# Kernel optimization log

Measured on AMD Instinct MI355X. Metric: run time of the kernel, lower is better.

The kernel has to match this reference:

```python
import jax, jax.numpy as jnp
import numpy as np

EMB = 1024
HEADS = 16
HEAD_DIM = EMB // HEADS
N = 16384


def setup_inputs() -> dict:
    key = jax.random.key(0)
    ks = jax.random.split(key, 9)
    s = 1.0 / np.sqrt(EMB)
    return {
        "src": jax.random.normal(ks[0], (N, EMB), dtype=jnp.float32),
        "Wq": jax.random.normal(ks[1], (EMB, EMB), dtype=jnp.float32) * s,
        "bq": jax.random.normal(ks[2], (EMB,), dtype=jnp.float32) * s,
        "Wk": jax.random.normal(ks[3], (EMB, EMB), dtype=jnp.float32) * s,
        "bk": jax.random.normal(ks[4], (EMB,), dtype=jnp.float32) * s,
        "Wv": jax.random.normal(ks[5], (EMB, EMB), dtype=jnp.float32) * s,
        "bv": jax.random.normal(ks[6], (EMB,), dtype=jnp.float32) * s,
        "Wo": jax.random.normal(ks[7], (EMB, EMB), dtype=jnp.float32) * s,
        "bo": jax.random.normal(ks[8], (EMB,), dtype=jnp.float32) * s,
    }


def reference(src, Wq, bq, Wk, bk, Wv, bv, Wo, bo):
    # nn.Linear: y = x @ W^T + b  (W is [out, in])
    q = src @ Wq.T + bq          # [N, E]
    k = src @ Wk.T + bk
    v = src @ Wv.T + bv
    q = q.reshape(-1, HEADS, HEAD_DIM)   # [N, H, D]
    k = k.reshape(-1, HEADS, HEAD_DIM)
    v = v.reshape(-1, HEADS, HEAD_DIM)
    # NOTE: attention is across heads within each token: scores [N, H, H]
    scale = 1.0 / jnp.sqrt(jnp.float32(HEAD_DIM))
    scores = jnp.einsum('nhd,ngd->nhg', q, k) * scale   # [N, H, H]
    attn = jax.nn.softmax(scores, axis=-1)
    out = jnp.einsum('nhg,ngd->nhd', attn, v)            # [N, H, D]
    out = out.reshape(-1, EMB)
    out = out @ Wo.T + bo                                 # [N, E]
    return out.reshape(-1, HEADS, HEAD_DIM)               # [N, H, D]
```

## Files before the change

kernel.cpp:

```cpp
#include <hip/hip_runtime.h>
#include <stdint.h>
#include <stddef.h>

#define EMB 1024
#define NTOK 16384

typedef __attribute__((ext_vector_type(8))) short short8;
typedef __attribute__((ext_vector_type(4))) float floatx4;

__device__ __forceinline__ unsigned short f2bf(float f) {
    union { float f; unsigned int u; } v; v.f = f;
    unsigned int u = v.u;
    unsigned int r = (u + 0x7fffu + ((u >> 16) & 1u)) >> 16;
    return (unsigned short)r;
}
__device__ __forceinline__ float bf2f(unsigned short s) {
    union { unsigned int u; float f; } v; v.u = ((unsigned int)s) << 16;
    return v.f;
}

__device__ __forceinline__ void gload16(const void* g, void* l) {
    __builtin_amdgcn_global_load_lds(
        (const __attribute__((address_space(1))) void*)g,
        (__attribute__((address_space(3))) void*)l, 16, 0, 0);
}

__global__ void cvt_kernel(const float* __restrict__ in,
                           unsigned short* __restrict__ out, int n4) {
    int idx = blockIdx.x * blockDim.x + threadIdx.x;
    int stride = gridDim.x * blockDim.x;
    for (int i = idx; i < n4; i += stride) {
        float4 f = reinterpret_cast<const float4*>(in)[i];
        ushort4 o;
        o.x = f2bf(f.x); o.y = f2bf(f.y); o.z = f2bf(f.z); o.w = f2bf(f.w);
        reinterpret_cast<ushort4*>(out)[i] = o;
    }
}

__global__ void cvt4_kernel(const float* __restrict__ s0, const float* __restrict__ s1,
                            const float* __restrict__ s2, const float* __restrict__ s3,
                            unsigned short* __restrict__ out) {
    int idx = blockIdx.x * blockDim.x + threadIdx.x;
    const int total = 4 << 18;
    int stride = gridDim.x * blockDim.x;
    for (int i = idx; i < total; i += stride) {
        int w = i >> 18, r = i & ((1 << 18) - 1);
        const float* s = (w == 0) ? s0 : (w == 1) ? s1 : (w == 2) ? s2 : s3;
        float4 f = reinterpret_cast<const float4*>(s)[r];
        ushort4 o;
        o.x = f2bf(f.x); o.y = f2bf(f.y); o.z = f2bf(f.z); o.w = f2bf(f.w);
        reinterpret_cast<ushort4*>(out)[i] = o;
    }
}

__global__ void bias_cat_kernel(const float* __restrict__ b0,
                                const float* __restrict__ b1,
                                const float* __restrict__ b2,
                                float* __restrict__ out) {
    int i = blockIdx.x * blockDim.x + threadIdx.x;
    float v = (i < 1024) ? b0[i] : (i < 2048 ? b1[i - 1024] : b2[i - 2048]);
    out[i] = v;
}

__device__ __forceinline__ void store_val(float* C, size_t idx, float v) { C[idx] = v; }
__device__ __forceinline__ void store_val(unsigned short* C, size_t idx, float v) { C[idx] = f2bf(v); }

template<typename OUT_T>
__global__ __launch_bounds__(512, 1)
void gemm256mn(const unsigned short* __restrict__ A,
               const unsigned short* __restrict__ B,
               const float* __restrict__ bias,
               OUT_T* __restrict__ C,
               int Nc, int nt_n)
{
    __shared__ unsigned short lds[65536];
    const int K = 1024;
    const int NT = 16;

    const int bid = blockIdx.x;
    const int x = bid & 7;
    const int w = bid >> 3;
    const int m0 = (x * 8 + (w & 7)) * 256;
    const int n_base = (w >> 3) * nt_n * 256;

    const int tid  = threadIdx.x;
    const int lane = tid & 63;
    const int wid  = tid >> 6;
    const int wm = (wid >> 2) * 128;
    const int wn = (wid & 3) * 64;
    const int rr = lane & 15;
    const int klo = (((lane >> 4) ^ ((rr >> 1) & 3)) << 3);

    const int aro = (wm + rr) * 32 + klo;
    const int bro = 16384 + (wn + rr) * 32 + klo;

    const unsigned short* pA[2];
    const unsigned short* pB[2];
    int ldst[2];
#pragma unroll
    for (int l = 0; l < 2; ++l) {
        const int P16  = l * 512 + tid;
        const int rowS = P16 >> 2;
        const int colel = (((P16 & 3) ^ ((rowS >> 1) & 3)) << 3);
        pA[l] = A + (size_t)(m0 + rowS) * K + colel;
        pB[l] = B + (size_t)(n_base + rowS) * K + colel;
        ldst[l] = P16 * 8;
    }
    const size_t nstep = (size_t)256 * K;

    floatx4 acc[8][4];
#pragma unroll
    for (int i = 0; i < 8; ++i)
#pragma unroll
        for (int j = 0; j < 4; ++j)
            acc[i][j] = (floatx4){0.f, 0.f, 0.f, 0.f};

    const int TOT = nt_n * NT;

#pragma unroll
    for (int l = 0; l < 2; ++l) {
        gload16(pA[l],      &lds[0     + ldst[l]]);
        gload16(pA[l] + 32, &lds[8192  + ldst[l]]);
        gload16(pB[l],      &lds[16384 + ldst[l]]);
        gload16(pB[l] + 32, &lds[24576 + ldst[l]]);
    }
    asm volatile("s_waitcnt vmcnt(0)" ::: "memory");
    asm volatile("s_barrier" ::: "memory");

    short8 a0[4], a1[4], b0[4];
#pragma unroll
    for (int i = 0; i < 4; ++i)
        a0[i] = *reinterpret_cast<const short8*>(&lds[aro + i * 512]);
#pragma unroll
    for (int j = 0; j < 4; ++j)
        b0[j] = *reinterpret_cast<const short8*>(&lds[bro + j * 512]);

    const int cn  = lane & 15;
    const int cm4 = (lane >> 4) * 4;

    for (int vt = 0; vt < TOT; ++vt) {
        const int cur = (vt & 1) * 32768;
        const int nxt = cur ^ 32768;
        int vtn = vt + 1; if (vtn == TOT) vtn = 0;
        const int ktn = (vtn & 15) * 64;
        const int nbn = vtn >> 4;
        const unsigned short* pBn0 = pB[0] + (size_t)nbn * nstep + ktn;
        const unsigned short* pBn1 = pB[1] + (size_t)nbn * nstep + ktn;

        gload16(pA[0] + ktn, &lds[nxt + ldst[0]]);
        gload16(pA[1] + ktn, &lds[nxt + ldst[1]]);
        gload16(pBn0,        &lds[nxt + 16384 + ldst[0]]);
        gload16(pBn1,        &lds[nxt + 16384 + ldst[1]]);
#pragma unroll
        for (int i = 0; i < 4; ++i)
            a1[i] = *reinterpret_cast<const short8*>(&lds[cur + aro + 2048 + i * 512]);
        __builtin_amdgcn_s_setprio(1);
#pragma unroll
        for (int j = 0; j < 4; ++j)
#pragma unroll
            for (int i = 0; i < 4; ++i)
                acc[i][j] = __builtin_amdgcn_mfma_f32_16x16x32_bf16(a0[i], b0[j], acc[i][j], 0, 0, 0);
#pragma unroll
        for (int j = 0; j < 4; ++j)
#pragma unroll
            for (int i = 0; i < 4; ++i)
                acc[4 + i][j] = __builtin_amdgcn_mfma_f32_16x16x32_bf16(a1[i], b0[j], acc[4 + i][j], 0, 0, 0);
        __builtin_amdgcn_s_setprio(0);
        asm volatile("s_waitcnt vmcnt(4)" ::: "memory");
        asm volatile("s_barrier" ::: "memory");

        gload16(pA[0] + ktn + 32, &lds[nxt + 8192 + ldst[0]]);
        gload16(pA[1] + ktn + 32, &lds[nxt + 8192 + ldst[1]]);
        gload16(pBn0 + 32,        &lds[nxt + 24576 + ldst[0]]);
        gload16(pBn1 + 32,        &lds[nxt + 24576 + ldst[1]]);
#pragma unroll
        for (int i = 0; i < 4; ++i)
            a0[i] = *reinterpret_cast<const short8*>(&lds[cur + 8192 + aro + i * 512]);
#pragma unroll
        for (int j = 0; j < 4; ++j)
            b0[j] = *reinterpret_cast<const short8*>(&lds[cur + 8192 + bro + j * 512]);
#pragma unroll
        for (int i = 0; i < 4; ++i)
            a1[i] = *reinterpret_cast<const short8*>(&lds[cur + 8192 + aro + 2048 + i * 512]);
        __builtin_amdgcn_s_setprio(1);
#pragma unroll
        for (int j = 0; j < 4; ++j)
#pragma unroll
            for (int i = 0; i < 4; ++i)
                acc[i][j] = __builtin_amdgcn_mfma_f32_16x16x32_bf16(a0[i], b0[j], acc[i][j], 0, 0, 0);
#pragma unroll
        for (int j = 0; j < 4; ++j)
#pragma unroll
            for (int i = 0; i < 4; ++i)
                acc[4 + i][j] = __builtin_amdgcn_mfma_f32_16x16x32_bf16(a1[i], b0[j], acc[4 + i][j], 0, 0, 0);
        __builtin_amdgcn_s_setprio(0);
        asm volatile("s_waitcnt vmcnt(4)" ::: "memory");
        asm volatile("s_barrier" ::: "memory");
#pragma unroll
        for (int i = 0; i < 4; ++i)
            a0[i] = *reinterpret_cast<const short8*>(&lds[nxt + aro + i * 512]);
#pragma unroll
        for (int j = 0; j < 4; ++j)
            b0[j] = *reinterpret_cast<const short8*>(&lds[nxt + bro + j * 512]);

        if ((vt & 15) == 15) {
            const int n0 = n_base + (vt >> 4) * 256;
            float bv[4];
#pragma unroll
            for (int j = 0; j < 4; ++j) bv[j] = bias[n0 + wn + j * 16 + cn];
#pragma unroll
            for (int ai = 0; ai < 8; ++ai) {
                const int row = m0 + wm + (ai >> 2) * 64 + (ai & 3) * 16 + cm4;
#pragma unroll
                for (int j = 0; j < 4; ++j) {
                    const int col = n0 + wn + j * 16 + cn;
#pragma unroll
                    for (int r = 0; r < 4; ++r)
                        store_val(C, (size_t)(row + r) * Nc + col, acc[ai][j][r] + bv[j]);
                }
            }
#pragma unroll
            for (int i = 0; i < 8; ++i)
#pragma unroll
                for (int j = 0; j < 4; ++j)
                    acc[i][j] = (floatx4){0.f, 0.f, 0.f, 0.f};
        }
    }
}

#define ROWP 72

__global__ __launch_bounds__(256)
void attn_kernel(const unsigned short* __restrict__ QKV,
                 unsigned short* __restrict__ O)
{
    const int wave = threadIdx.x >> 6;
    const int lane = threadIdx.x & 63;
    const int n = blockIdx.x * 4 + wave;

    __shared__ unsigned short lq[4][16 * ROWP];
    __shared__ unsigned short lk[4][16 * ROWP];
    __shared__ unsigned short lv[4][16 * ROWP];
    __shared__ float lp[4][256];

    {
        const unsigned short* gq = QKV + (size_t)n * 3072;
        const unsigned short* gk = gq + 1024;
        const unsigned short* gv = gq + 2048;
        for (int t = lane; t < 128; t += 64) {
            int r = t >> 3, c = t & 7;
            *reinterpret_cast<short8*>(&lq[wave][r * ROWP + c * 8]) =
                *reinterpret_cast<const short8*>(gq + t * 8);
            *reinterpret_cast<short8*>(&lk[wave][r * ROWP + c * 8]) =
                *reinterpret_cast<const short8*>(gk + t * 8);
            *reinterpret_cast<short8*>(&lv[wave][r * ROWP + c * 8]) =
                *reinterpret_cast<const short8*>(gv + t * 8);
        }
    }
    __syncthreads();

    const int g = lane & 15;
    const int a = lane >> 4;

    float kf[64];
#pragma unroll
    for (int c2 = 0; c2 < 8; ++c2) {
        short8 kv = *reinterpret_cast<const short8*>(&lk[wave][g * ROWP + c2 * 8]);
#pragma unroll
        for (int e = 0; e < 8; ++e) kf[c2 * 8 + e] = bf2f((unsigned short)kv[e]);
    }

#pragma unroll
    for (int i = 0; i < 4; ++i) {
        const int h = i * 4 + a;
        float s = 0.f;
#pragma unroll
        for (int c2 = 0; c2 < 8; ++c2) {
            short8 qv = *reinterpret_cast<const short8*>(&lq[wave][h * ROWP + c2 * 8]);
#pragma unroll
            for (int e = 0; e < 8; ++e)
                s = fmaf(bf2f((unsigned short)qv[e]), kf[c2 * 8 + e], s);
        }
        s *= 0.125f;

        float m = s;
#pragma unroll
        for (int o = 1; o < 16; o <<= 1) m = fmaxf(m, __shfl_xor(m, o, 64));
        float p = expf(s - m);
        float sum = p;
#pragma unroll
        for (int o = 1; o < 16; o <<= 1) sum += __shfl_xor(sum, o, 64);
        lp[wave][h * 16 + g] = p / sum;
    }
    __syncthreads();

    const int h = lane >> 2;
    const int db = (lane & 3) * 16;
    float o[16];
#pragma unroll
    for (int e = 0; e < 16; ++e) o[e] = 0.f;

    for (int g2 = 0; g2 < 16; ++g2) {
        const float pw = lp[wave][h * 16 + g2];
        short8 v0 = *reinterpret_cast<const short8*>(&lv[wave][g2 * ROWP + db]);
        short8 v1 = *reinterpret_cast<const short8*>(&lv[wave][g2 * ROWP + db + 8]);
#pragma unroll
        for (int e = 0; e < 8; ++e) {
            o[e]     = fmaf(pw, bf2f((unsigned short)v0[e]), o[e]);
            o[8 + e] = fmaf(pw, bf2f((unsigned short)v1[e]), o[8 + e]);
        }
    }

    short8 o0, o1;
#pragma unroll
    for (int e = 0; e < 8; ++e) {
        o0[e] = (short)f2bf(o[e]);
        o1[e] = (short)f2bf(o[8 + e]);
    }
    unsigned short* dst = O + (size_t)n * EMB + h * 64 + db;
    *reinterpret_cast<short8*>(dst) = o0;
    *reinterpret_cast<short8*>(dst + 8) = o1;
}

extern "C" void kernel_launch(void* const* d_in, const int* in_sizes, int n_in,
                              void* d_out, int out_size, void* d_ws, size_t ws_size,
                              hipStream_t stream)
{
    const float* src = (const float*)d_in[0];
    const float* Wq  = (const float*)d_in[1];
    const float* bq  = (const float*)d_in[2];
    const float* Wk  = (const float*)d_in[3];
    const float* bk  = (const float*)d_in[4];
    const float* Wv  = (const float*)d_in[5];
    const float* bv  = (const float*)d_in[6];
    const float* Wo  = (const float*)d_in[7];
    const float* bo  = (const float*)d_in[8];
    float* out = (float*)d_out;

    unsigned short* ws = (unsigned short*)d_ws;
    unsigned short* src_bf = ws;
    unsigned short* wqkv   = src_bf + (size_t)NTOK * EMB;
    unsigned short* wo_bf  = wqkv + (size_t)3 * EMB * EMB;
    unsigned short* qkv    = wo_bf + (size_t)EMB * EMB;
    unsigned short* ab     = qkv + (size_t)NTOK * 3 * EMB;
    float* bias_cat        = (float*)(ab + (size_t)NTOK * EMB);

    cvt_kernel<<<2048, 256, 0, stream>>>(src, src_bf, NTOK * EMB / 4);
    cvt4_kernel<<<2048, 256, 0, stream>>>(Wq, Wk, Wv, Wo, wqkv);
    bias_cat_kernel<<<12, 256, 0, stream>>>(bq, bk, bv, bias_cat);

    gemm256mn<unsigned short><<<dim3(256), 512, 0, stream>>>(
        src_bf, wqkv, bias_cat, qkv, 3 * EMB, 3);

    attn_kernel<<<NTOK / 4, 256, 0, stream>>>(qkv, ab);

    gemm256mn<float><<<dim3(256), 512, 0, stream>>>(
        ab, wo_bf, bo, out, EMB, 1);
}
```

Baseline: 201.2 us.

## Restructure GEMM main loop into 4-stage 32-wide K pipeline with prefetch depth two

Replaces the double-buffered 64-wide K step, which was split into two 32-wide halves each with its own barrier, with a quad-buffered ring of 32-wide K slices. Global-to-LDS loads are issued two steps ahead, and each iteration reads all 8 A fragments at once. There is one wait and one barrier per 32-wide slice. The LDS swizzle and the row mapping of the accumulators change to match. The aim is to hide global-load latency behind more MFMA work and to simplify scheduling, at the cost of more live registers and more barriers per K element.

```diff
diff --git a/kernel.cpp b/kernel.cpp
--- a/kernel.cpp
+++ b/kernel.cpp
@@ -67,15 +67,14 @@
 
 template<typename OUT_T>
 __global__ __launch_bounds__(512, 1)
-void gemm256mn(const unsigned short* __restrict__ A,
-               const unsigned short* __restrict__ B,
-               const float* __restrict__ bias,
-               OUT_T* __restrict__ C,
-               int Nc, int nt_n)
+void gemm32q(const unsigned short* __restrict__ A,
+             const unsigned short* __restrict__ B,
+             const float* __restrict__ bias,
+             OUT_T* __restrict__ C,
+             int Nc, int nt_n)
 {
     __shared__ unsigned short lds[65536];
     const int K = 1024;
-    const int NT = 16;
 
     const int bid = blockIdx.x;
     const int x = bid & 7;
@@ -83,30 +82,20 @@
     const int m0 = (x * 8 + (w & 7)) * 256;
     const int n_base = (w >> 3) * nt_n * 256;
 
-    const int tid  = threadIdx.x;
-    const int lane = tid & 63;
-    const int wid  = tid >> 6;
-    const int wm = (wid >> 2) * 128;
-    const int wn = (wid & 3) * 64;
-    const int rr = lane & 15;
-    const int klo = (((lane >> 4) ^ ((rr >> 1) & 3)) << 3);
-
-    const int aro = (wm + rr) * 32 + klo;
-    const int bro = 16384 + (wn + rr) * 32 + klo;
-
-    const unsigned short* pA[2];
-    const unsigned short* pB[2];
-    int ldst[2];
-#pragma unroll
-    for (int l = 0; l < 2; ++l) {
-        const int P16  = l * 512 + tid;
-        const int rowS = P16 >> 2;
-        const int colel = (((P16 & 3) ^ ((rowS >> 1) & 3)) << 3);
-        pA[l] = A + (size_t)(m0 + rowS) * K + colel;
-        pB[l] = B + (size_t)(n_base + rowS) * K + colel;
-        ldst[l] = P16 * 8;
-    }
+    const int tid = threadIdx.x, lane = tid & 63, wid = tid >> 6;
+    const int wm = (wid >> 2) * 128, wn = (wid & 3) * 64;
+    const int rr = lane & 15, ls = lane >> 4;
+    const int swf = ((ls ^ (rr & 3)) << 3);
+    const int arE = (wm + rr) * 32 + swf;
+    const int brE = 8192 + (wn + rr) * 32 + swf;
+
+    const int rowT = tid >> 2;
+    const int colT = (((tid & 3) ^ (rowT & 3)) << 3);
+    const unsigned short* pA0 = A + (size_t)(m0 + rowT) * K + colT;
+    const unsigned short* pB0 = B + (size_t)(n_base + rowT) * K + colT;
+    const size_t half  = (size_t)128 * K;
     const size_t nstep = (size_t)256 * K;
+    const int ldA = tid * 8, ldB = 8192 + tid * 8;
 
     floatx4 acc[8][4];
 #pragma unroll
@@ -115,108 +104,69 @@
         for (int j = 0; j < 4; ++j)
             acc[i][j] = (floatx4){0.f, 0.f, 0.f, 0.f};
 
-    const int TOT = nt_n * NT;
-
-#pragma unroll
-    for (int l = 0; l < 2; ++l) {
-        gload16(pA[l],      &lds[0     + ldst[l]]);
-        gload16(pA[l] + 32, &lds[8192  + ldst[l]]);
-        gload16(pB[l],      &lds[16384 + ldst[l]]);
-        gload16(pB[l] + 32, &lds[24576 + ldst[l]]);
-    }
-    asm volatile("s_waitcnt vmcnt(0)" ::: "memory");
-    asm volatile("s_barrier" ::: "memory");
-
-    short8 a0[4], a1[4], b0[4];
-#pragma unroll
-    for (int i = 0; i < 4; ++i)
-        a0[i] = *reinterpret_cast<const short8*>(&lds[aro + i * 512]);
-#pragma unroll
-    for (int j = 0; j < 4; ++j)
-        b0[j] = *reinterpret_cast<const short8*>(&lds[bro + j * 512]);
-
+    const int TOT = nt_n * 32;
     const int cn  = lane & 15;
     const int cm4 = (lane >> 4) * 4;
 
+    gload16(pA0,          &lds[ldA]);
+    gload16(pA0 + half,   &lds[ldA + 4096]);
+    gload16(pB0,          &lds[ldB]);
+    gload16(pB0 + half,   &lds[ldB + 4096]);
+    gload16(pA0 + 32,          &lds[16384 + ldA]);
+    gload16(pA0 + half + 32,   &lds[16384 + ldA + 4096]);
+    gload16(pB0 + 32,          &lds[16384 + ldB]);
+    gload16(pB0 + half + 32,   &lds[16384 + ldB + 4096]);
+    asm volatile("s_waitcnt vmcnt(4)" ::: "memory");
+    asm volatile("s_barrier" ::: "memory");
+
+#pragma unroll 4
     for (int vt = 0; vt < TOT; ++vt) {
-        const int cur = (vt & 1) * 32768;
-        const int nxt = cur ^ 32768;
-        int vtn = vt + 1; if (vtn == TOT) vtn = 0;
-        const int ktn = (vtn & 15) * 64;
-        const int nbn = vtn >> 4;
-        const unsigned short* pBn0 = pB[0] + (size_t)nbn * nstep + ktn;
-        const unsigned short* pBn1 = pB[1] + (size_t)nbn * nstep + ktn;
-
-        gload16(pA[0] + ktn, &lds[nxt + ldst[0]]);
-        gload16(pA[1] + ktn, &lds[nxt + ldst[1]]);
-        gload16(pBn0,        &lds[nxt + 16384 + ldst[0]]);
-        gload16(pBn1,        &lds[nxt + 16384 + ldst[1]]);
-#pragma unroll
-        for (int i = 0; i < 4; ++i)
-            a1[i] = *reinterpret_cast<const short8*>(&lds[cur + aro + 2048 + i * 512]);
+        const int bufr = (vt & 3) * 16384;
+
+        short8 a[8], b[4];
+#pragma unroll
+        for (int i = 0; i < 8; ++i)
+            a[i] = *reinterpret_cast<const short8*>(&lds[bufr + arE + i * 512]);
+#pragma unroll
+        for (int j = 0; j < 4; ++j)
+            b[j] = *reinterpret_cast<const short8*>(&lds[bufr + brE + j * 512]);
+
+        {
+            int t2 = vt + 2; if (t2 >= TOT) t2 -= TOT;
+            const int buf2 = (t2 & 3) * 16384;
+            const int kt2  = (t2 & 31) * 32;
+            const unsigned short* pBn = pB0 + (size_t)(t2 >> 5) * nstep + kt2;
+            gload16(pA0 + kt2,        &lds[buf2 + ldA]);
+            gload16(pA0 + half + kt2, &lds[buf2 + ldA + 4096]);
+            gload16(pBn,              &lds[buf2 + ldB]);
+            gload16(pBn + half,       &lds[buf2 + ldB + 4096]);
+        }
+
         __builtin_amdgcn_s_setprio(1);
 #pragma unroll
         for (int j = 0; j < 4; ++j)
 #pragma unroll
-            for (int i = 0; i < 4; ++i)
-                acc[i][j] = __builtin_amdgcn_mfma_f32_16x16x32_bf16(a0[i], b0[j], acc[i][j], 0, 0, 0);
-#pragma unroll
-        for (int j = 0; j < 4; ++j)
-#pragma unroll
-            for (int i = 0; i < 4; ++i)
-                acc[4 + i][j] = __builtin_amdgcn_mfma_f32_16x16x32_bf16(a1[i], b0[j], acc[4 + i][j], 0, 0, 0);
+            for (int i = 0; i < 8; ++i)
+                acc[i][j] = __builtin_amdgcn_mfma_f32_16x16x32_bf16(a[i], b[j], acc[i][j], 0, 0, 0);
         __builtin_amdgcn_s_setprio(0);
+
         asm volatile("s_waitcnt vmcnt(4)" ::: "memory");
         asm volatile("s_barrier" ::: "memory");
 
-        gload16(pA[0] + ktn + 32, &lds[nxt + 8192 + ldst[0]]);
-        gload16(pA[1] + ktn + 32, &lds[nxt + 8192 + ldst[1]]);
-        gload16(pBn0 + 32,        &lds[nxt + 24576 + ldst[0]]);
-        gload16(pBn1 + 32,        &lds[nxt + 24576 + ldst[1]]);
-#pragma unroll
-        for (int i = 0; i < 4; ++i)
-            a0[i] = *reinterpret_cast<const short8*>(&lds[cur + 8192 + aro + i * 512]);
-#pragma unroll
-        for (int j = 0; j < 4; ++j)
-            b0[j] = *reinterpret_cast<const short8*>(&lds[cur + 8192 + bro + j * 512]);
-#pragma unroll
-        for (int i = 0; i < 4; ++i)
-            a1[i] = *reinterpret_cast<const short8*>(&lds[cur + 8192 + aro + 2048 + i * 512]);
-        __builtin_amdgcn_s_setprio(1);
-#pragma unroll
-        for (int j = 0; j < 4; ++j)
-#pragma unroll
-            for (int i = 0; i < 4; ++i)
-                acc[i][j] = __builtin_amdgcn_mfma_f32_16x16x32_bf16(a0[i], b0[j], acc[i][j], 0, 0, 0);
-#pragma unroll
-        for (int j = 0; j < 4; ++j)
-#pragma unroll
-            for (int i = 0; i < 4; ++i)
-                acc[4 + i][j] = __builtin_amdgcn_mfma_f32_16x16x32_bf16(a1[i], b0[j], acc[4 + i][j], 0, 0, 0);
-        __builtin_amdgcn_s_setprio(0);
-        asm volatile("s_waitcnt vmcnt(4)" ::: "memory");
-        asm volatile("s_barrier" ::: "memory");
-#pragma unroll
-        for (int i = 0; i < 4; ++i)
-            a0[i] = *reinterpret_cast<const short8*>(&lds[nxt + aro + i * 512]);
-#pragma unroll
-        for (int j = 0; j < 4; ++j)
-            b0[j] = *reinterpret_cast<const short8*>(&lds[nxt + bro + j * 512]);
-
-        if ((vt & 15) == 15) {
-            const int n0 = n_base + (vt >> 4) * 256;
+        if ((vt & 31) == 31) {
+            const int n0 = n_base + (vt >> 5) * 256;
             float bv[4];
 #pragma unroll
             for (int j = 0; j < 4; ++j) bv[j] = bias[n0 + wn + j * 16 + cn];
 #pragma unroll
-            for (int ai = 0; ai < 8; ++ai) {
-                const int row = m0 + wm + (ai >> 2) * 64 + (ai & 3) * 16 + cm4;
+            for (int i = 0; i < 8; ++i) {
+                const int row = m0 + wm + i * 16 + cm4;
 #pragma unroll
                 for (int j = 0; j < 4; ++j) {
                     const int col = n0 + wn + j * 16 + cn;
 #pragma unroll
                     for (int r = 0; r < 4; ++r)
-                        store_val(C, (size_t)(row + r) * Nc + col, acc[ai][j][r] + bv[j]);
+                        store_val(C, (size_t)(row + r) * Nc + col, acc[i][j][r] + bv[j]);
                 }
             }
 #pragma unroll
@@ -349,11 +299,11 @@
     cvt4_kernel<<<2048, 256, 0, stream>>>(Wq, Wk, Wv, Wo, wqkv);
     bias_cat_kernel<<<12, 256, 0, stream>>>(bq, bk, bv, bias_cat);
 
-    gemm256mn<unsigned short><<<dim3(256), 512, 0, stream>>>(
+    gemm32q<unsigned short><<<dim3(256), 512, 0, stream>>>(
         src_bf, wqkv, bias_cat, qkv, 3 * EMB, 3);
 
     attn_kernel<<<NTOK / 4, 256, 0, stream>>>(qkv, ab);
 
-    gemm256mn<float><<<dim3(256), 512, 0, stream>>>(
+    gemm32q<float><<<dim3(256), 512, 0, stream>>>(
         ab, wo_bf, bo, out, EMB, 1);
 }
```

After: 200.1 us. About the same (-0.5%).

## Fuse src fp32-to-bf16 conversion into QKV GEMM A-tile loading

Applied to the files above, without the earlier changes.

The QKV projection GEMM now reads the fp32 input directly and converts it to bf16 in registers before writing the A tile to LDS. This removes the standalone conversion pass over the whole activation and its bf16 scratch buffer. The bias concatenation is folded into the weight-conversion kernel, which saves one launch. The trade-off is that A is loaded through registers rather than the direct global-to-LDS path, and the fp32 A traffic is re-read for each output column tile.

```diff
diff --git a/kernel.cpp b/kernel.cpp
--- a/kernel.cpp
+++ b/kernel.cpp
@@ -25,21 +25,21 @@
         (__attribute__((address_space(3))) void*)l, 16, 0, 0);
 }
 
-__global__ void cvt_kernel(const float* __restrict__ in,
-                           unsigned short* __restrict__ out, int n4) {
-    int idx = blockIdx.x * blockDim.x + threadIdx.x;
-    int stride = gridDim.x * blockDim.x;
-    for (int i = idx; i < n4; i += stride) {
-        float4 f = reinterpret_cast<const float4*>(in)[i];
-        ushort4 o;
-        o.x = f2bf(f.x); o.y = f2bf(f.y); o.z = f2bf(f.z); o.w = f2bf(f.w);
-        reinterpret_cast<ushort4*>(out)[i] = o;
-    }
-}
-
-__global__ void cvt4_kernel(const float* __restrict__ s0, const float* __restrict__ s1,
-                            const float* __restrict__ s2, const float* __restrict__ s3,
-                            unsigned short* __restrict__ out) {
+#define SB0() __builtin_amdgcn_sched_barrier(0)
+
+__global__ void cvtwb_kernel(const float* __restrict__ s0, const float* __restrict__ s1,
+                             const float* __restrict__ s2, const float* __restrict__ s3,
+                             const float* __restrict__ b0, const float* __restrict__ b1,
+                             const float* __restrict__ b2,
+                             unsigned short* __restrict__ out, float* __restrict__ bias_cat) {
+    if (blockIdx.x == 0) {
+#pragma unroll
+        for (int t = 0; t < 12; ++t) {
+            int i = t * 256 + threadIdx.x;
+            float v = (i < 1024) ? b0[i] : (i < 2048 ? b1[i - 1024] : b2[i - 2048]);
+            bias_cat[i] = v;
+        }
+    }
     int idx = blockIdx.x * blockDim.x + threadIdx.x;
     const int total = 4 << 18;
     int stride = gridDim.x * blockDim.x;
@@ -53,17 +53,214 @@
     }
 }
 
-__global__ void bias_cat_kernel(const float* __restrict__ b0,
-                                const float* __restrict__ b1,
-                                const float* __restrict__ b2,
-                                float* __restrict__ out) {
-    int i = blockIdx.x * blockDim.x + threadIdx.x;
-    float v = (i < 1024) ? b0[i] : (i < 2048 ? b1[i - 1024] : b2[i - 2048]);
-    out[i] = v;
-}
-
 __device__ __forceinline__ void store_val(float* C, size_t idx, float v) { C[idx] = v; }
 __device__ __forceinline__ void store_val(unsigned short* C, size_t idx, float v) { C[idx] = f2bf(v); }
+
+__global__ __launch_bounds__(512, 1)
+void gemmA32(const float* __restrict__ Afp,
+             const unsigned short* __restrict__ B,
+             const float* __restrict__ bias,
+             unsigned short* __restrict__ C,
+             int Nc, int nt_n)
+{
+    __shared__ unsigned short lds[65536];
+    const int K = 1024;
+
+    const int bid = blockIdx.x;
+    const int x = bid & 7;
+    const int w = bid >> 3;
+    const int m0 = (x * 8 + (w & 7)) * 256;
+    const int n_base = (w >> 3) * nt_n * 256;
+
+    const int tid  = threadIdx.x;
+    const int lane = tid & 63;
+    const int wid  = tid >> 6;
+    const int wm = (wid >> 2) * 128;
+    const int wn = (wid & 3) * 64;
+    const int rr = lane & 15;
+    const int klo = (((lane >> 4) ^ ((rr >> 1) & 3)) << 3);
+
+    const int aro = (wm + rr) * 32 + klo;
+    const int bro = 16384 + (wn + rr) * 32 + klo;
+
+    const float* pAf[2];
+    const unsigned short* pB[2];
+    int ldst[2];
+#pragma unroll
+    for (int l = 0; l < 2; ++l) {
+        const int P16  = l * 512 + tid;
+        const int rowS = P16 >> 2;
+        const int colel = (((P16 & 3) ^ ((rowS >> 1) & 3)) << 3);
+        pAf[l] = Afp + (size_t)(m0 + rowS) * K + colel;
+        pB[l]  = B + (size_t)(n_base + rowS) * K + colel;
+        ldst[l] = P16 * 8;
+    }
+    const size_t nstep = (size_t)256 * K;
+
+    floatx4 acc[8][4];
+#pragma unroll
+    for (int i = 0; i < 8; ++i)
+#pragma unroll
+        for (int j = 0; j < 4; ++j)
+            acc[i][j] = (floatx4){0.f, 0.f, 0.f, 0.f};
+
+    const int NT = 16;
+    const int TOT = nt_n * NT;
+
+#pragma unroll
+    for (int l = 0; l < 2; ++l) {
+#pragma unroll
+        for (int kh = 0; kh < 2; ++kh) {
+            float4 f0 = *reinterpret_cast<const float4*>(pAf[l] + kh * 32);
+            float4 f1 = *reinterpret_cast<const float4*>(pAf[l] + kh * 32 + 4);
+            short8 o;
+            o[0] = (short)f2bf(f0.x); o[1] = (short)f2bf(f0.y);
+            o[2] = (short)f2bf(f0.z); o[3] = (short)f2bf(f0.w);
+            o[4] = (short)f2bf(f1.x); o[5] = (short)f2bf(f1.y);
+            o[6] = (short)f2bf(f1.z); o[7] = (short)f2bf(f1.w);
+            *reinterpret_cast<short8*>(&lds[kh * 8192 + ldst[l]]) = o;
+        }
+        gload16(pB[l],      &lds[16384 + ldst[l]]);
+        gload16(pB[l] + 32, &lds[24576 + ldst[l]]);
+    }
+    asm volatile("s_waitcnt vmcnt(0)" ::: "memory");
+    asm volatile("s_waitcnt lgkmcnt(0)" ::: "memory");
+    asm volatile("s_barrier" ::: "memory");
+
+    short8 a0[4], a1[4], b0[4];
+#pragma unroll
+    for (int i = 0; i < 4; ++i)
+        a0[i] = *reinterpret_cast<const short8*>(&lds[aro + i * 512]);
+#pragma unroll
+    for (int j = 0; j < 4; ++j)
+        b0[j] = *reinterpret_cast<const short8*>(&lds[bro + j * 512]);
+
+    const int cn  = lane & 15;
+    const int cm4 = (lane >> 4) * 4;
+
+    for (int vt = 0; vt < TOT; ++vt) {
+        const int cur = (vt & 1) * 32768;
+        const int nxt = cur ^ 32768;
+        int vtn = vt + 1; if (vtn == TOT) vtn = 0;
+        const int ktn = (vtn & 15) * 64;
+        const int nbn = vtn >> 4;
+        const unsigned short* pBn0 = pB[0] + (size_t)nbn * nstep + ktn;
+        const unsigned short* pBn1 = pB[1] + (size_t)nbn * nstep + ktn;
+
+        float4 fA00 = *reinterpret_cast<const float4*>(pAf[0] + ktn);
+        float4 fA01 = *reinterpret_cast<const float4*>(pAf[0] + ktn + 4);
+        float4 fA10 = *reinterpret_cast<const float4*>(pAf[1] + ktn);
+        float4 fA11 = *reinterpret_cast<const float4*>(pAf[1] + ktn + 4);
+        gload16(pBn0, &lds[nxt + 16384 + ldst[0]]);
+        gload16(pBn1, &lds[nxt + 16384 + ldst[1]]);
+#pragma unroll
+        for (int i = 0; i < 4; ++i)
+            a1[i] = *reinterpret_cast<const short8*>(&lds[cur + aro + 2048 + i * 512]);
+        __builtin_amdgcn_s_setprio(1);
+#pragma unroll
+        for (int j = 0; j < 4; ++j)
+#pragma unroll
+            for (int i = 0; i < 4; ++i)
+                acc[i][j] = __builtin_amdgcn_mfma_f32_16x16x32_bf16(a0[i], b0[j], acc[i][j], 0, 0, 0);
+#pragma unroll
+        for (int j = 0; j < 4; ++j)
+#pragma unroll
+            for (int i = 0; i < 4; ++i)
+                acc[4 + i][j] = __builtin_amdgcn_mfma_f32_16x16x32_bf16(a1[i], b0[j], acc[4 + i][j], 0, 0, 0);
+        __builtin_amdgcn_s_setprio(0);
+        SB0();
+        {
+            short8 o0, o1;
+            o0[0] = (short)f2bf(fA00.x); o0[1] = (short)f2bf(fA00.y);
+            o0[2] = (short)f2bf(fA00.z); o0[3] = (short)f2bf(fA00.w);
+            o0[4] = (short)f2bf(fA01.x); o0[5] = (short)f2bf(fA01.y);
+            o0[6] = (short)f2bf(fA01.z); o0[7] = (short)f2bf(fA01.w);
+            o1[0] = (short)f2bf(fA10.x); o1[1] = (short)f2bf(fA10.y);
+            o1[2] = (short)f2bf(fA10.z); o1[3] = (short)f2bf(fA10.w);
+            o1[4] = (short)f2bf(fA11.x); o1[5] = (short)f2bf(fA11.y);
+            o1[6] = (short)f2bf(fA11.z); o1[7] = (short)f2bf(fA11.w);
+            *reinterpret_cast<short8*>(&lds[nxt + ldst[0]]) = o0;
+            *reinterpret_cast<short8*>(&lds[nxt + ldst[1]]) = o1;
+        }
+        asm volatile("s_waitcnt vmcnt(2)" ::: "memory");
+        asm volatile("s_waitcnt lgkmcnt(0)" ::: "memory");
+        asm volatile("s_barrier" ::: "memory");
+
+        fA00 = *reinterpret_cast<const float4*>(pAf[0] + ktn + 32);
+        fA01 = *reinterpret_cast<const float4*>(pAf[0] + ktn + 36);
+        fA10 = *reinterpret_cast<const float4*>(pAf[1] + ktn + 32);
+        fA11 = *reinterpret_cast<const float4*>(pAf[1] + ktn + 36);
+        gload16(pBn0 + 32, &lds[nxt + 24576 + ldst[0]]);
+        gload16(pBn1 + 32, &lds[nxt + 24576 + ldst[1]]);
+#pragma unroll
+        for (int i = 0; i < 4; ++i)
+            a0[i] = *reinterpret_cast<const short8*>(&lds[cur + 8192 + aro + i * 512]);
+#pragma unroll
+        for (int j = 0; j < 4; ++j)
+            b0[j] = *reinterpret_cast<const short8*>(&lds[cur + 8192 + bro + j * 512]);
+#pragma unroll
+        for (int i = 0; i < 4; ++i)
+            a1[i] = *reinterpret_cast<const short8*>(&lds[cur + 8192 + aro + 2048 + i * 512]);
+        __builtin_amdgcn_s_setprio(1);
+#pragma unroll
+        for (int j = 0; j < 4; ++j)
+#pragma unroll
+            for (int i = 0; i < 4; ++i)
+                acc[i][j] = __builtin_amdgcn_mfma_f32_16x16x32_bf16(a0[i], b0[j], acc[i][j], 0, 0, 0);
+#pragma unroll
+        for (int j = 0; j < 4; ++j)
+#pragma unroll
+            for (int i = 0; i < 4; ++i)
+                acc[4 + i][j] = __builtin_amdgcn_mfma_f32_16x16x32_bf16(a1[i], b0[j], acc[4 + i][j], 0, 0, 0);
+        __builtin_amdgcn_s_setprio(0);
+        SB0();
+        {
+            short8 o0, o1;
+            o0[0] = (short)f2bf(fA00.x); o0[1] = (short)f2bf(fA00.y);
+            o0[2] = (short)f2bf(fA00.z); o0[3] = (short)f2bf(fA00.w);
+            o0[4] = (short)f2bf(fA01.x); o0[5] = (short)f2bf(fA01.y);
+            o0[6] = (short)f2bf(fA01.z); o0[7] = (short)f2bf(fA01.w);
+            o1[0] = (short)f2bf(fA10.x); o1[1] = (short)f2bf(fA10.y);
+            o1[2] = (short)f2bf(fA10.z); o1[3] = (short)f2bf(fA10.w);
+            o1[4] = (short)f2bf(fA11.x); o1[5] = (short)f2bf(fA11.y);
+            o1[6] = (short)f2bf(fA11.z); o1[7] = (short)f2bf(fA11.w);
+            *reinterpret_cast<short8*>(&lds[nxt + 8192 + ldst[0]]) = o0;
+            *reinterpret_cast<short8*>(&lds[nxt + 8192 + ldst[1]]) = o1;
+        }
+        asm volatile("s_waitcnt vmcnt(2)" ::: "memory");
+        asm volatile("s_waitcnt lgkmcnt(0)" ::: "memory");
+        asm volatile("s_barrier" ::: "memory");
+#pragma unroll
+        for (int i = 0; i < 4; ++i)
+            a0[i] = *reinterpret_cast<const short8*>(&lds[nxt + aro + i * 512]);
+#pragma unroll
+        for (int j = 0; j < 4; ++j)
+            b0[j] = *reinterpret_cast<const short8*>(&lds[nxt + bro + j * 512]);
+
+        if ((vt & 15) == 15) {
+            const int n0 = n_base + (vt >> 4) * 256;
+            float bv[4];
+#pragma unroll
+            for (int j = 0; j < 4; ++j) bv[j] = bias[n0 + wn + j * 16 + cn];
+#pragma unroll
+            for (int ai = 0; ai < 8; ++ai) {
+                const int row = m0 + wm + (ai >> 2) * 64 + (ai & 3) * 16 + cm4;
+#pragma unroll
+                for (int j = 0; j < 4; ++j) {
+                    const int col = n0 + wn + j * 16 + cn;
+#pragma unroll
+                    for (int r = 0; r < 4; ++r)
+                        C[(size_t)(row + r) * Nc + col] = f2bf(acc[ai][j][r] + bv[j]);
+                }
+            }
+#pragma unroll
+            for (int i = 0; i < 8; ++i)
+#pragma unroll
+                for (int j = 0; j < 4; ++j)
+                    acc[i][j] = (floatx4){0.f, 0.f, 0.f, 0.f};
+        }
+    }
+}
 
 template<typename OUT_T>
 __global__ __launch_bounds__(512, 1)
@@ -338,22 +535,17 @@
     float* out = (float*)d_out;
 
     unsigned short* ws = (unsigned short*)d_ws;
-    unsigned short* src_bf = ws;
-    unsigned short* wqkv   = src_bf + (size_t)NTOK * EMB;
+    unsigned short* wqkv   = ws;
     unsigned short* wo_bf  = wqkv + (size_t)3 * EMB * EMB;
     unsigned short* qkv    = wo_bf + (size_t)EMB * EMB;
     unsigned short* ab     = qkv + (size_t)NTOK * 3 * EMB;
     float* bias_cat        = (float*)(ab + (size_t)NTOK * EMB);
 
-    cvt_kernel<<<2048, 256, 0, stream>>>(src, src_bf, NTOK * EMB / 4);
-    cvt4_kernel<<<2048, 256, 0, stream>>>(Wq, Wk, Wv, Wo, wqkv);
-    bias_cat_kernel<<<12, 256, 0, stream>>>(bq, bk, bv, bias_cat);
-
-    gemm256mn<unsigned short><<<dim3(256), 512, 0, stream>>>(
-        src_bf, wqkv, bias_cat, qkv, 3 * EMB, 3);
+    cvtwb_kernel<<<2048, 256, 0, stream>>>(Wq, Wk, Wv, Wo, bq, bk, bv, wqkv, bias_cat);
+
+    gemmA32<<<dim3(256), 512, 0, stream>>>(src, wqkv, bias_cat, qkv, 3 * EMB, 3);
 
     attn_kernel<<<NTOK / 4, 256, 0, stream>>>(qkv, ab);
 
-    gemm256mn<float><<<dim3(256), 512, 0, stream>>>(
-        ab, wo_bf, bo, out, EMB, 1);
-}
+    gemm256mn<float><<<dim3(256), 512, 0, stream>>>(ab, wo_bf, bo, out, EMB, 1);
+}
```

Measured after the change: 227.1 us. 1.13x slower.
